# Kernel optimization log

Measured on AMD Instinct MI355X. Metric: run time of the kernel, lower is better.

## Reference

```python
import jax, jax.numpy as jnp
import numpy as np

EMBED_DIM = 768
M, C = 8192, 4096
NEG_SAMPLES = 2   # args.neg_sample
CL_TEMP = 1.0
P_INF = 1000.0
EPS = 1e-8


def exp_map0(x, curv):
    # Lorentz exponential map at the origin (space components only, MERU-style).
    rc_xnorm = jnp.sqrt(curv) * jnp.linalg.norm(x, axis=-1, keepdims=True)
    return jnp.sinh(rc_xnorm) * x / jnp.maximum(rc_xnorm, EPS)


def pairwise_dist(x, y, curv):
    # x: (m, d) space components, y: (c, d); Lorentz geodesic distance.
    x_time = jnp.sqrt(1.0 / curv + jnp.sum(x * x, axis=-1))   # (m,)
    y_time = jnp.sqrt(1.0 / curv + jnp.sum(y * y, axis=-1))   # (c,)
    inner = x @ y.T - x_time[:, None] * y_time[None, :]        # Lorentz inner product (m, c)
    cd = jnp.maximum(-curv * inner, 1.0 + EPS)
    return jnp.arccosh(cd) / jnp.sqrt(curv)


def setup_inputs() -> dict:
    key = jax.random.key(0)
    k1, k2, k3 = jax.random.split(key, 3)
    return {
        "text_embeddings": jax.random.normal(k1, (M, EMBED_DIM), dtype=jnp.float32),
        "label_embeddings": jax.random.normal(k2, (C, EMBED_DIM), dtype=jnp.float32),
        "target_labels": jax.random.randint(k3, (M,), 0, C),
        "curv_log": jnp.float32(np.log(1.0)),                      # curv param (log-space)
        "text_alpha_log": jnp.float32(np.log(EMBED_DIM ** -0.5)),  # text_alpha (log-space)
        "label_alpha_log": jnp.float32(np.log(EMBED_DIM ** -0.5)), # label_alpha (log-space)
    }


def reference(text_embeddings, label_embeddings, target_labels, curv_log, text_alpha_log, label_alpha_log):
    curv = jnp.exp(curv_log)
    te = text_embeddings * jnp.exp(text_alpha_log)
    le = label_embeddings * jnp.exp(label_alpha_log)
    text_hyp = exp_map0(te, curv)
    label_hyp = exp_map0(le, curv)
    dist = pairwise_dist(text_hyp, label_hyp, curv)        # (m, c)
    m = dist.shape[0]
    rows = jnp.arange(m)
    # hard-negative mining: mask out the positive label, take k smallest distances
    masked = dist.at[rows, target_labels].set(P_INF)
    neg_minus_dist, _ = jax.lax.top_k(-masked, NEG_SAMPLES)  # (m, k) = -dist of hardest negatives
    neg_scores = neg_minus_dist / CL_TEMP                     # -dist / temp
    pos_score = -dist[rows, target_labels] / CL_TEMP          # (m,)
    denom = jnp.exp(pos_score) + jnp.sum(jnp.exp(neg_scores), axis=-1)
    loss = jnp.log(denom) - pos_score                         # = -log(exp(pos)/denom)
    return loss                                               # (m,) per-sample losses
```

## Files before the change

### kernel.cpp

```cpp
#include <hip/hip_runtime.h>
#include <hip/hip_bf16.h>
#include <math.h>

#define MM 8192
#define CC 4096
#define DD 768
#define EPSF 1e-8f

#define BM 256
#define BN 256
#define BK 64
#define TPB 512
#define NKT (DD / BK)
#define NROWT (MM / BM)
#define NCOLT (CC / BN)

#define XB_OFF 0
#define YB_OFF (MM * DD * 2)
#define FW_OFF (YB_OFF + CC * DD * 2)
#define S_T 0
#define T_T (MM)
#define S_L (2 * MM)
#define T_L (2 * MM + CC)
#define CA_T (2 * MM + 2 * CC)
#define POS  (CA_T + MM)
#define PART (POS + MM)

typedef __attribute__((ext_vector_type(8))) short short8;
typedef __attribute__((ext_vector_type(4))) unsigned short u16x4;
typedef __attribute__((ext_vector_type(4))) float f32x4;

__device__ inline unsigned short f2bf(float f) {
    unsigned int u = __float_as_uint(f);
    u += 0x7FFF + ((u >> 16) & 1);
    return (unsigned short)(u >> 16);
}

__device__ inline void gll16(const void* g, void* l) {
    __builtin_amdgcn_global_load_lds(
        (const __attribute__((address_space(1))) void*)(uintptr_t)g,
        (__attribute__((address_space(3))) void*)(unsigned)(uintptr_t)l,
        16, 0, 0);
}

#define BAR() do { __builtin_amdgcn_sched_barrier(0); __builtin_amdgcn_s_barrier(); __builtin_amdgcn_sched_barrier(0); } while (0)
#define VM8 asm volatile("s_waitcnt vmcnt(8)" ::: "memory")
#define VM6 asm volatile("s_waitcnt vmcnt(6)" ::: "memory")
#define VM4 asm volatile("s_waitcnt vmcnt(4)" ::: "memory")
#define VM0 asm volatile("s_waitcnt vmcnt(0)" ::: "memory")
#define NOPS ((void)0)

#define DSR(dst, base, off) \
    asm volatile("ds_read_b128 %0, %1 offset:%c2" : "=v"(dst) : "v"(base), "n"(off))

#define MFMA_B(a, b, c) __builtin_amdgcn_mfma_f32_16x16x32_bf16((a), (b), (c), 0, 0, 0)

__global__ void prep_conv_kernel(const float* __restrict__ X, const float* __restrict__ Y,
                                 const float* curv_log, const float* ta_log, const float* la_log,
                                 char* __restrict__ wsb) {
    unsigned short* Xb = (unsigned short*)(wsb + XB_OFF);
    unsigned short* Yb = (unsigned short*)(wsb + YB_OFF);
    float* fws = (float*)(wsb + FW_OFF);
    int wid = threadIdx.x >> 6, lane = threadIdx.x & 63;
    int row = blockIdx.x * 4 + wid;
    float curv = __expf(curv_log[0]);
    const float* src; unsigned short* dst; float alpha; int idx; int is_text;
    if (row < MM) {
        src = X + (size_t)row * DD; dst = Xb + (size_t)row * DD;
        alpha = __expf(ta_log[0]); idx = row; is_text = 1;
    } else {
        int r = row - MM;
        src = Y + (size_t)r * DD; dst = Yb + (size_t)r * DD;
        alpha = __expf(la_log[0]); idx = r; is_text = 0;
    }
    float n2 = 0.f;
    #pragma unroll
    for (int j = 0; j < 3; ++j) {
        float4 v = *(const float4*)(src + lane * 4 + 256 * j);
        n2 += v.x * v.x + v.y * v.y + v.z * v.z + v.w * v.w;
        u16x4 o; o[0] = f2bf(v.x); o[1] = f2bf(v.y); o[2] = f2bf(v.z); o[3] = f2bf(v.w);
        *(u16x4*)(dst + lane * 4 + 256 * j) = o;
    }
    #pragma unroll
    for (int m = 32; m; m >>= 1) n2 += __shfl_xor(n2, m);
    if (lane == 0) {
        float r = sqrtf(curv) * alpha * sqrtf(n2);
        float s = alpha * sinhf(r) / fmaxf(r, EPSF);
        float tt = sqrtf(1.0f / curv + s * s * n2);
        if (is_text) {
            fws[S_T + idx] = s; fws[T_T + idx] = tt; fws[CA_T + idx] = tt / s;
        } else {
            fws[S_L + idx] = s; fws[T_L + idx] = tt;
        }
    }
}

__global__ void pos_kernel(const float* __restrict__ X, const float* __restrict__ Y,
                           const int* __restrict__ tgt, const float* curv_log,
                           char* __restrict__ wsb) {
    float* fws = (float*)(wsb + FW_OFF);
    int wid = threadIdx.x >> 6, lane = threadIdx.x & 63;
    int row = blockIdx.x * 4 + wid;
    if (row >= MM) return;
    float curv = __expf(curv_log[0]);
    int t = tgt[row];
    const float* xr = X + (size_t)row * DD;
    const float* yr = Y + (size_t)t * DD;
    float dot = 0.f;
    #pragma unroll
    for (int k = 0; k < DD / 64; ++k) dot += xr[lane + 64 * k] * yr[lane + 64 * k];
    #pragma unroll
    for (int m = 32; m; m >>= 1) dot += __shfl_xor(dot, m);
    if (lane == 0) {
        float inner = fws[S_T + row] * fws[S_L + t] * dot - fws[T_T + row] * fws[T_L + t];
        float cd = fmaxf(-curv * inner, 1.0f + EPSF);
        float d = __logf(cd + sqrtf(cd * cd - 1.0f)) * rsqrtf(curv);
        fws[POS + row] = d;
    }
}

__global__ __launch_bounds__(TPB) void main_kernel(
    const int* __restrict__ tgt, char* __restrict__ wsb)
{
    __shared__ unsigned short Ald[4 * 8192];
    __shared__ unsigned short Bld[4 * 8192];
    __shared__ float red[256][4][2];

    const unsigned short* Xb = (const unsigned short*)(wsb + XB_OFF);
    const unsigned short* Yb = (const unsigned short*)(wsb + YB_OFF);
    float* fws = (float*)(wsb + FW_OFF);

    int tid = threadIdx.x;
    int lane = tid & 63, wid = tid >> 6;
    int wr = wid >> 2, wc = wid & 3;
    int l15 = lane & 15, rgrp = lane >> 4;

    int bid = blockIdx.x;
    int pos = bid >> 3;
    int coltile = pos >> 2;
    int rowpanel = (bid & 7) * 4 + (pos & 3);
    int rowbase = rowpanel * BM;
    int colbase = coltile * BN;

    int ko_src = ((tid & 3) ^ ((tid >> 3) & 3)) * 8;
    const unsigned short* xk = Xb + (size_t)(rowbase + (tid >> 2)) * DD + ko_src;
    const unsigned short* yk = Yb + (size_t)(colbase + (tid >> 2)) * DD + ko_src;
    unsigned short* adst = Ald + tid * 8;
    unsigned short* bdst = Bld + tid * 8;

#define STG_A(OFF, RG) do { gll16(xk + (OFF), adst + (RG) * 8192); \
                            gll16(xk + (size_t)128 * DD + (OFF), adst + (RG) * 8192 + 4096); } while (0)
#define STG_B(OFF, RG) do { gll16(yk + (OFF), bdst + (RG) * 8192); \
                            gll16(yk + (size_t)128 * DD + (OFF), bdst + (RG) * 8192 + 4096); } while (0)

    unsigned a_base = (unsigned)(uintptr_t)(&Ald[0]) + (wr * 128 + l15) * 64
                      + ((rgrp * 16) ^ (((l15 >> 1) & 3) << 4));
    unsigned b_base = (unsigned)(uintptr_t)(&Bld[0]) + (wc * 64 + l15) * 64
                      + ((rgrp * 16) ^ (((l15 >> 1) & 3) << 4));

    f32x4 acc[8][4];
    #pragma unroll
    for (int a = 0; a < 8; ++a)
        #pragma unroll
        for (int b = 0; b < 4; ++b)
            acc[a][b] = (f32x4){0.f, 0.f, 0.f, 0.f};

    short8 afE[4], afO[4], bf0[4], bf1[4];

#define LDA(S, RG, MH) do { \
    DSR(S[0], a_base, (RG) * 16384 + ((MH) * 4 + 0) * 1024); \
    DSR(S[1], a_base, (RG) * 16384 + ((MH) * 4 + 1) * 1024); \
    DSR(S[2], a_base, (RG) * 16384 + ((MH) * 4 + 2) * 1024); \
    DSR(S[3], a_base, (RG) * 16384 + ((MH) * 4 + 3) * 1024); } while (0)
#define LDB(S, RG) do { \
    DSR(S[0], b_base, (RG) * 16384 + 0); \
    DSR(S[1], b_base, (RG) * 16384 + 1024); \
    DSR(S[2], b_base, (RG) * 16384 + 2048); \
    DSR(S[3], b_base, (RG) * 16384 + 3072); } while (0)

#define MF16(AF, BF, AO) do { \
    acc[(AO)+0][0] = MFMA_B(AF[0], BF[0], acc[(AO)+0][0]); \
    acc[(AO)+0][1] = MFMA_B(AF[0], BF[1], acc[(AO)+0][1]); \
    acc[(AO)+0][2] = MFMA_B(AF[0], BF[2], acc[(AO)+0][2]); \
    acc[(AO)+0][3] = MFMA_B(AF[0], BF[3], acc[(AO)+0][3]); \
    acc[(AO)+1][0] = MFMA_B(AF[1], BF[0], acc[(AO)+1][0]); \
    acc[(AO)+1][1] = MFMA_B(AF[1], BF[1], acc[(AO)+1][1]); \
    acc[(AO)+1][2] = MFMA_B(AF[1], BF[2], acc[(AO)+1][2]); \
    acc[(AO)+1][3] = MFMA_B(AF[1], BF[3], acc[(AO)+1][3]); \
    acc[(AO)+2][0] = MFMA_B(AF[2], BF[0], acc[(AO)+2][0]); \
    acc[(AO)+2][1] = MFMA_B(AF[2], BF[1], acc[(AO)+2][1]); \
    acc[(AO)+2][2] = MFMA_B(AF[2], BF[2], acc[(AO)+2][2]); \
    acc[(AO)+2][3] = MFMA_B(AF[2], BF[3], acc[(AO)+2][3]); \
    acc[(AO)+3][0] = MFMA_B(AF[3], BF[0], acc[(AO)+3][0]); \
    acc[(AO)+3][1] = MFMA_B(AF[3], BF[1], acc[(AO)+3][1]); \
    acc[(AO)+3][2] = MFMA_B(AF[3], BF[2], acc[(AO)+3][2]); \
    acc[(AO)+3][3] = MFMA_B(AF[3], BF[3], acc[(AO)+3][3]); \
} while (0)

#define PH(LD, STG, W, LGN, MF) do { \
    LD; \
    STG; \
    W; \
    BAR(); \
    asm volatile("s_waitcnt lgkmcnt(" #LGN ")" ::: "memory"); \
    __builtin_amdgcn_sched_barrier(0); \
    __builtin_amdgcn_s_setprio(1); \
    MF; \
    __builtin_amdgcn_s_setprio(0); \
    BAR(); \
} while (0)

    STG_A(0, 0);  STG_B(0, 0);
    STG_A(32, 1); STG_B(32, 1);
    STG_A(64, 2); STG_B(64, 2);
    VM8;
    BAR();
    LDB(bf0, 0); LDA(afE, 0, 0);

    #pragma unroll 1
    for (int kp = 0; kp < 5; ++kp) {
        PH(LDA(afO, 0, 1),               STG_A(96, 3),  VM6, 4, MF16(afE, bf0, 0));
        PH(LDB(bf1, 1); LDA(afE, 1, 0),  STG_B(96, 3),  VM6, 8, MF16(afO, bf0, 4));
        PH(LDA(afO, 1, 1),               STG_A(128, 0), VM6, 4, MF16(afE, bf1, 0));
        PH(LDB(bf0, 2); LDA(afE, 2, 0),  STG_B(128, 0), VM6, 8, MF16(afO, bf1, 4));
        PH(LDA(afO, 2, 1),               STG_A(160, 1), VM6, 4, MF16(afE, bf0, 0));
        PH(LDB(bf1, 3); LDA(afE, 3, 0),  STG_B(160, 1), VM6, 8, MF16(afO, bf0, 4));
        PH(LDA(afO, 3, 1),               STG_A(192, 2), VM6, 4, MF16(afE, bf1, 0));
        PH(LDB(bf0, 0); LDA(afE, 0, 0),  STG_B(192, 2), VM6, 8, MF16(afO, bf1, 4));
        xk += 128; yk += 128;
    }
    PH(LDA(afO, 0, 1),               STG_A(96, 3), VM6, 4, MF16(afE, bf0, 0));
    PH(LDB(bf1, 1); LDA(afE, 1, 0),  STG_B(96, 3), VM6, 8, MF16(afO, bf0, 4));
    PH(LDA(afO, 1, 1),               NOPS, VM4, 4, MF16(afE, bf1, 0));
    PH(LDB(bf0, 2); LDA(afE, 2, 0),  NOPS, VM0, 8, MF16(afO, bf1, 4));
    PH(LDA(afO, 2, 1),               NOPS, NOPS, 4, MF16(afE, bf0, 0));
    PH(LDB(bf1, 3); LDA(afE, 3, 0),  NOPS, NOPS, 8, MF16(afO, bf0, 4));
    PH(LDA(afO, 3, 1),               NOPS, NOPS, 4, MF16(afE, bf1, 0));
    PH(NOPS,                         NOPS, NOPS, 0, MF16(afO, bf1, 4));

    int colb = colbase + wc * 64 + l15;
    float sbv[4], tbv[4];
    #pragma unroll
    for (int nf = 0; nf < 4; ++nf) { sbv[nf] = fws[S_L + colb + nf * 16]; tbv[nf] = fws[T_L + colb + nf * 16]; }

    float m1[32], m2[32];
    #pragma unroll
    for (int mf = 0; mf < 8; ++mf) {
        int rw = rowbase + wr * 128 + mf * 16 + rgrp * 4;
        #pragma unroll
        for (int j = 0; j < 4; ++j) {
            float ca = fws[CA_T + rw + j];
            int tgj = tgt[rw + j];
            float a = -3.4e38f, b = -3.4e38f;
            #pragma unroll
            for (int nf = 0; nf < 4; ++nf) {
                float u = sbv[nf] * acc[mf][nf][j] - ca * tbv[nf];
                if (colb + nf * 16 == tgj) u = -3.4e38f;
                float n1 = fmaxf(a, u);
                b = fmaxf(b, fminf(a, u));
                a = n1;
            }
            m1[mf * 4 + j] = a; m2[mf * 4 + j] = b;
        }
    }
    #pragma unroll
    for (int mask = 1; mask <= 8; mask <<= 1)
        #pragma unroll
        for (int i = 0; i < 32; ++i) {
            float o1 = __shfl_xor(m1[i], mask);
            float o2 = __shfl_xor(m2[i], mask);
            float n1 = fmaxf(m1[i], o1);
            m2[i] = fmaxf(fminf(m1[i], o1), fmaxf(m2[i], o2));
            m1[i] = n1;
        }
    if (l15 == 0) {
        #pragma unroll
        for (int mf = 0; mf < 8; ++mf)
            #pragma unroll
            for (int j = 0; j < 4; ++j) {
                int rl = wr * 128 + mf * 16 + rgrp * 4 + j;
                red[rl][wc][0] = m1[mf * 4 + j];
                red[rl][wc][1] = m2[mf * 4 + j];
            }
    }
    __syncthreads();
    if (tid < 256) {
        float p1 = -3.4e38f, p2 = -3.4e38f;
        #pragma unroll
        for (int g = 0; g < 4; ++g) {
            float a1 = red[tid][g][0], a2 = red[tid][g][1];
            float n1 = fmaxf(p1, a1);
            p2 = fmaxf(fminf(p1, a1), fmaxf(p2, a2));
            p1 = n1;
        }
        int row = rowbase + tid;
        fws[PART + ((size_t)row * NCOLT + coltile) * 2 + 0] = p1;
        fws[PART + ((size_t)row * NCOLT + coltile) * 2 + 1] = p2;
    }
}

__global__ void final_kernel(const char* __restrict__ wsb, const float* __restrict__ curv_log,
                             float* __restrict__ out) {
    const float* fws = (const float*)(wsb + FW_OFF);
    int row = blockIdx.x * 256 + threadIdx.x;
    if (row >= MM) return;
    float curv = __expf(curv_log[0]);
    float rsc = rsqrtf(curv);
    const float* p = fws + PART + (size_t)row * (NCOLT * 2);
    float p1 = -3.4e38f, p2 = -3.4e38f;
    #pragma unroll
    for (int s = 0; s < NCOLT; ++s) {
        float a1 = p[s * 2], a2 = p[s * 2 + 1];
        float n1 = fmaxf(p1, a1);
        p2 = fmaxf(fminf(p1, a1), fmaxf(p2, a2));
        p1 = n1;
    }
    float sa = fws[S_T + row];
    float i1 = sa * p1, i2 = sa * p2;
    float cd1 = fmaxf(-curv * i1, 1.0f + EPSF);
    float d1 = __logf(cd1 + sqrtf(cd1 * cd1 - 1.0f)) * rsc;
    float cd2 = fmaxf(-curv * i2, 1.0f + EPSF);
    float d2 = __logf(cd2 + sqrtf(cd2 * cd2 - 1.0f)) * rsc;
    float dp = fws[POS + row];
    float denom = __expf(-dp) + __expf(-d1) + __expf(-d2);
    out[row] = __logf(denom) + dp;
}

extern "C" void kernel_launch(void* const* d_in, const int* in_sizes, int n_in,
                              void* d_out, int out_size, void* d_ws, size_t ws_size,
                              hipStream_t stream) {
    const float* X = (const float*)d_in[0];
    const float* Y = (const float*)d_in[1];
    const int* tgt = (const int*)d_in[2];
    const float* curv_log = (const float*)d_in[3];
    const float* ta_log = (const float*)d_in[4];
    const float* la_log = (const float*)d_in[5];
    char* wsb = (char*)d_ws;
    float* out = (float*)d_out;

    prep_conv_kernel<<<(MM + CC) / 4, 256, 0, stream>>>(X, Y, curv_log, ta_log, la_log, wsb);
    pos_kernel<<<MM / 4, 256, 0, stream>>>(X, Y, tgt, curv_log, wsb);
    main_kernel<<<NROWT * NCOLT, TPB, 0, stream>>>(tgt, wsb);
    final_kernel<<<MM / 256, 256, 0, stream>>>(wsb, curv_log, out);
}
```

Baseline: 88.58 us.

## Restructure GEMM main loop into four 32-MFMA phases with combined A/B staging

The K-loop pipeline is rebuilt so each phase issues A and B global->LDS loads together, waits, barriers, then issues all 12 LDS fragment reads for the next k-step and runs 32 MFMAs on the previous fragments. This halves the number of barriers per k-step and doubles the MFMA work between syncs, at the cost of more live fragment registers (8 A fragments per buffer). The prep kernel also remaps blocks so text-row conversion is interleaved across the row space, changing the write/launch order of rows.

```diff
diff --git a/kernel.cpp b/kernel.cpp
--- a/kernel.cpp
+++ b/kernel.cpp
@@ -45,7 +45,6 @@
 
 #define BAR() do { __builtin_amdgcn_sched_barrier(0); __builtin_amdgcn_s_barrier(); __builtin_amdgcn_sched_barrier(0); } while (0)
 #define VM8 asm volatile("s_waitcnt vmcnt(8)" ::: "memory")
-#define VM6 asm volatile("s_waitcnt vmcnt(6)" ::: "memory")
 #define VM4 asm volatile("s_waitcnt vmcnt(4)" ::: "memory")
 #define VM0 asm volatile("s_waitcnt vmcnt(0)" ::: "memory")
 #define NOPS ((void)0)
@@ -62,7 +61,10 @@
     unsigned short* Yb = (unsigned short*)(wsb + YB_OFF);
     float* fws = (float*)(wsb + FW_OFF);
     int wid = threadIdx.x >> 6, lane = threadIdx.x & 63;
-    int row = blockIdx.x * 4 + wid;
+    int b = blockIdx.x;
+    int row;
+    if (b < MM / 4) row = (b & 7) * 1024 + (b >> 3) * 4 + wid;
+    else            row = b * 4 + wid;
     float curv = __expf(curv_log[0]);
     const float* src; unsigned short* dst; float alpha; int idx; int is_text;
     if (row < MM) {
@@ -148,10 +150,11 @@
     unsigned short* adst = Ald + tid * 8;
     unsigned short* bdst = Bld + tid * 8;
 
-#define STG_A(OFF, RG) do { gll16(xk + (OFF), adst + (RG) * 8192); \
-                            gll16(xk + (size_t)128 * DD + (OFF), adst + (RG) * 8192 + 4096); } while (0)
-#define STG_B(OFF, RG) do { gll16(yk + (OFF), bdst + (RG) * 8192); \
-                            gll16(yk + (size_t)128 * DD + (OFF), bdst + (RG) * 8192 + 4096); } while (0)
+#define STG_AB(OFF, RG) do { \
+    gll16(xk + (OFF), adst + (RG) * 8192); \
+    gll16(xk + (size_t)128 * DD + (OFF), adst + (RG) * 8192 + 4096); \
+    gll16(yk + (OFF), bdst + (RG) * 8192); \
+    gll16(yk + (size_t)128 * DD + (OFF), bdst + (RG) * 8192 + 4096); } while (0)
 
     unsigned a_base = (unsigned)(uintptr_t)(&Ald[0]) + (wr * 128 + l15) * 64
                       + ((rgrp * 16) ^ (((l15 >> 1) & 3) << 4));
@@ -165,43 +168,36 @@
         for (int b = 0; b < 4; ++b)
             acc[a][b] = (f32x4){0.f, 0.f, 0.f, 0.f};
 
-    short8 afE[4], afO[4], bf0[4], bf1[4];
-
-#define LDA(S, RG, MH) do { \
-    DSR(S[0], a_base, (RG) * 16384 + ((MH) * 4 + 0) * 1024); \
-    DSR(S[1], a_base, (RG) * 16384 + ((MH) * 4 + 1) * 1024); \
-    DSR(S[2], a_base, (RG) * 16384 + ((MH) * 4 + 2) * 1024); \
-    DSR(S[3], a_base, (RG) * 16384 + ((MH) * 4 + 3) * 1024); } while (0)
-#define LDB(S, RG) do { \
-    DSR(S[0], b_base, (RG) * 16384 + 0); \
-    DSR(S[1], b_base, (RG) * 16384 + 1024); \
-    DSR(S[2], b_base, (RG) * 16384 + 2048); \
-    DSR(S[3], b_base, (RG) * 16384 + 3072); } while (0)
-
-#define MF16(AF, BF, AO) do { \
-    acc[(AO)+0][0] = MFMA_B(AF[0], BF[0], acc[(AO)+0][0]); \
-    acc[(AO)+0][1] = MFMA_B(AF[0], BF[1], acc[(AO)+0][1]); \
-    acc[(AO)+0][2] = MFMA_B(AF[0], BF[2], acc[(AO)+0][2]); \
-    acc[(AO)+0][3] = MFMA_B(AF[0], BF[3], acc[(AO)+0][3]); \
-    acc[(AO)+1][0] = MFMA_B(AF[1], BF[0], acc[(AO)+1][0]); \
-    acc[(AO)+1][1] = MFMA_B(AF[1], BF[1], acc[(AO)+1][1]); \
-    acc[(AO)+1][2] = MFMA_B(AF[1], BF[2], acc[(AO)+1][2]); \
-    acc[(AO)+1][3] = MFMA_B(AF[1], BF[3], acc[(AO)+1][3]); \
-    acc[(AO)+2][0] = MFMA_B(AF[2], BF[0], acc[(AO)+2][0]); \
-    acc[(AO)+2][1] = MFMA_B(AF[2], BF[1], acc[(AO)+2][1]); \
-    acc[(AO)+2][2] = MFMA_B(AF[2], BF[2], acc[(AO)+2][2]); \
-    acc[(AO)+2][3] = MFMA_B(AF[2], BF[3], acc[(AO)+2][3]); \
-    acc[(AO)+3][0] = MFMA_B(AF[3], BF[0], acc[(AO)+3][0]); \
-    acc[(AO)+3][1] = MFMA_B(AF[3], BF[1], acc[(AO)+3][1]); \
-    acc[(AO)+3][2] = MFMA_B(AF[3], BF[2], acc[(AO)+3][2]); \
-    acc[(AO)+3][3] = MFMA_B(AF[3], BF[3], acc[(AO)+3][3]); \
-} while (0)
-
-#define PH(LD, STG, W, LGN, MF) do { \
-    LD; \
+    short8 afE[8], afO[8], bfE[4], bfO[4];
+
+#define LD12(AS, BS, RG) do { \
+    DSR(BS[0], b_base, (RG) * 16384 + 0); \
+    DSR(BS[1], b_base, (RG) * 16384 + 1024); \
+    DSR(BS[2], b_base, (RG) * 16384 + 2048); \
+    DSR(BS[3], b_base, (RG) * 16384 + 3072); \
+    DSR(AS[0], a_base, (RG) * 16384 + 0 * 1024); \
+    DSR(AS[1], a_base, (RG) * 16384 + 1 * 1024); \
+    DSR(AS[2], a_base, (RG) * 16384 + 2 * 1024); \
+    DSR(AS[3], a_base, (RG) * 16384 + 3 * 1024); \
+    DSR(AS[4], a_base, (RG) * 16384 + 4 * 1024); \
+    DSR(AS[5], a_base, (RG) * 16384 + 5 * 1024); \
+    DSR(AS[6], a_base, (RG) * 16384 + 6 * 1024); \
+    DSR(AS[7], a_base, (RG) * 16384 + 7 * 1024); } while (0)
+
+#define MF32(AF, BF) do { \
+    _Pragma("unroll") \
+    for (int mf = 0; mf < 8; ++mf) { \
+        acc[mf][0] = MFMA_B(AF[mf], BF[0], acc[mf][0]); \
+        acc[mf][1] = MFMA_B(AF[mf], BF[1], acc[mf][1]); \
+        acc[mf][2] = MFMA_B(AF[mf], BF[2], acc[mf][2]); \
+        acc[mf][3] = MFMA_B(AF[mf], BF[3], acc[mf][3]); \
+    } } while (0)
+
+#define PH(STG, W, LD, LGN, MF) do { \
     STG; \
     W; \
     BAR(); \
+    LD; \
     asm volatile("s_waitcnt lgkmcnt(" #LGN ")" ::: "memory"); \
     __builtin_amdgcn_sched_barrier(0); \
     __builtin_amdgcn_s_setprio(1); \
@@ -210,33 +206,23 @@
     BAR(); \
 } while (0)
 
-    STG_A(0, 0);  STG_B(0, 0);
-    STG_A(32, 1); STG_B(32, 1);
-    STG_A(64, 2); STG_B(64, 2);
+    STG_AB(0, 0); STG_AB(32, 1); STG_AB(64, 2);
     VM8;
     BAR();
-    LDB(bf0, 0); LDA(afE, 0, 0);
+    LD12(afE, bfE, 0);
 
     #pragma unroll 1
     for (int kp = 0; kp < 5; ++kp) {
-        PH(LDA(afO, 0, 1),               STG_A(96, 3),  VM6, 4, MF16(afE, bf0, 0));
-        PH(LDB(bf1, 1); LDA(afE, 1, 0),  STG_B(96, 3),  VM6, 8, MF16(afO, bf0, 4));
-        PH(LDA(afO, 1, 1),               STG_A(128, 0), VM6, 4, MF16(afE, bf1, 0));
-        PH(LDB(bf0, 2); LDA(afE, 2, 0),  STG_B(128, 0), VM6, 8, MF16(afO, bf1, 4));
-        PH(LDA(afO, 2, 1),               STG_A(160, 1), VM6, 4, MF16(afE, bf0, 0));
-        PH(LDB(bf1, 3); LDA(afE, 3, 0),  STG_B(160, 1), VM6, 8, MF16(afO, bf0, 4));
-        PH(LDA(afO, 3, 1),               STG_A(192, 2), VM6, 4, MF16(afE, bf1, 0));
-        PH(LDB(bf0, 0); LDA(afE, 0, 0),  STG_B(192, 2), VM6, 8, MF16(afO, bf1, 4));
+        PH(STG_AB(96, 3),  VM8, LD12(afO, bfO, 1), 12, MF32(afE, bfE));
+        PH(STG_AB(128, 0), VM8, LD12(afE, bfE, 2), 12, MF32(afO, bfO));
+        PH(STG_AB(160, 1), VM8, LD12(afO, bfO, 3), 12, MF32(afE, bfE));
+        PH(STG_AB(192, 2), VM8, LD12(afE, bfE, 0), 12, MF32(afO, bfO));
         xk += 128; yk += 128;
     }
-    PH(LDA(afO, 0, 1),               STG_A(96, 3), VM6, 4, MF16(afE, bf0, 0));
-    PH(LDB(bf1, 1); LDA(afE, 1, 0),  STG_B(96, 3), VM6, 8, MF16(afO, bf0, 4));
-    PH(LDA(afO, 1, 1),               NOPS, VM4, 4, MF16(afE, bf1, 0));
-    PH(LDB(bf0, 2); LDA(afE, 2, 0),  NOPS, VM0, 8, MF16(afO, bf1, 4));
-    PH(LDA(afO, 2, 1),               NOPS, NOPS, 4, MF16(afE, bf0, 0));
-    PH(LDB(bf1, 3); LDA(afE, 3, 0),  NOPS, NOPS, 8, MF16(afO, bf0, 4));
-    PH(LDA(afO, 3, 1),               NOPS, NOPS, 4, MF16(afE, bf1, 0));
-    PH(NOPS,                         NOPS, NOPS, 0, MF16(afO, bf1, 4));
+    PH(STG_AB(96, 3), VM8, LD12(afO, bfO, 1), 12, MF32(afE, bfE));
+    PH(NOPS,          VM4, LD12(afE, bfE, 2), 12, MF32(afO, bfO));
+    PH(NOPS,          VM0, LD12(afO, bfO, 3), 12, MF32(afE, bfE));
+    PH(NOPS,          NOPS, NOPS,              0, MF32(afO, bfO));
 
     int colb = colbase + wc * 64 + l15;
     float sbv[4], tbv[4];
```

Measured after the change: 113.5 us. 1.28x slower.
